# Optimization experiments

Hardware: AMD Instinct MI355X
Metric: run time of the kernel (lower is better)

Reference implementation:

```python
import jax, jax.numpy as jnp
import numpy as np

B, N, IN_DIM, OUT_DIM, H = 4, 2048, 1024, 1024, 16
HEAD_DIM = OUT_DIM // H  # 64


def setup_inputs() -> dict:
    key = jax.random.key(0)
    k_x, k_q, k_k, k_v, k_o = jax.random.split(key, 5)
    s = 1.0 / np.sqrt(IN_DIM)
    return {
        "x": jax.random.normal(k_x, (B, N, IN_DIM), dtype=jnp.float32),
        "w_q": jax.random.normal(k_q, (IN_DIM, OUT_DIM), dtype=jnp.float32) * s,
        "w_k": jax.random.normal(k_k, (IN_DIM, OUT_DIM), dtype=jnp.float32) * s,
        "w_v": jax.random.normal(k_v, (IN_DIM, OUT_DIM), dtype=jnp.float32) * s,
        "w_out": jax.random.normal(k_o, (OUT_DIM, OUT_DIM), dtype=jnp.float32) * s,
    }


def reference(x, w_q, w_k, w_v, w_out):
    b, n, _ = x.shape
    scale = 1.0 / jnp.sqrt(jnp.float32(HEAD_DIM))
    # QKV projections, split into heads: [b, h, n, d]
    q = (x @ w_q).reshape(b, n, H, HEAD_DIM).transpose(0, 2, 1, 3)
    k = (x @ w_k).reshape(b, n, H, HEAD_DIM).transpose(0, 2, 1, 3)
    v = (x @ w_v).reshape(b, n, H, HEAD_DIM).transpose(0, 2, 1, 3)
    # full score matrix [b, h, q, k]
    scores = jnp.einsum("bhqd,bhkd->bhqk", q, k) * scale
    # NOTE: source applies softmax over dim=1 (the HEAD axis) — reproduce exactly
    attn = jax.nn.softmax(scores, axis=1)
    # dropout p=0.0 -> identity
    ctx = jnp.einsum("bhqk,bhkd->bqhd", attn, v).reshape(b, n, OUT_DIM)
    return ctx @ w_out
```

## Files before the change

kernel.cpp:

```cpp
#include <hip/hip_runtime.h>
#include <hip/hip_bf16.h>

typedef unsigned short u16;
typedef unsigned int u32;
typedef __attribute__((ext_vector_type(8))) short short8;
typedef __attribute__((ext_vector_type(4))) float float4v;
typedef __attribute__((ext_vector_type(4))) unsigned int uint4v;

__device__ __forceinline__ u16 f2bf(float f) {
    union { float f; unsigned int u; } v; v.f = f;
    unsigned int r = v.u + 0x7fffu + ((v.u >> 16) & 1u);
    return (u16)(r >> 16);
}
__device__ __forceinline__ float bf2f(u16 h) {
    union { unsigned int u; float f; } v; v.u = ((unsigned int)h) << 16;
    return v.f;
}

__device__ __forceinline__ void gld_lds16(const u16* g, u16* l) {
    __builtin_amdgcn_global_load_lds(
        (const __attribute__((address_space(1))) u32*)g,
        (__attribute__((address_space(3))) u32*)l, 16, 0, 0);
}

__global__ __launch_bounds__(256) void convert_x(
    const float* __restrict__ x, u16* __restrict__ xb) {
    int i = (blockIdx.x * 256 + threadIdx.x) * 8;
    float4v a = *(const float4v*)&x[i];
    float4v b = *(const float4v*)&x[i + 4];
    u16 tmp[8] __attribute__((aligned(16)));
#pragma unroll
    for (int j = 0; j < 4; ++j) { tmp[j] = f2bf(a[j]); tmp[4 + j] = f2bf(b[j]); }
    *(uint4v*)&xb[i] = *(uint4v*)tmp;
}

__global__ __launch_bounds__(256) void transpose_w(
    const float* __restrict__ w0, const float* __restrict__ w1,
    const float* __restrict__ w2, const float* __restrict__ w3,
    u16* __restrict__ o0, u16* __restrict__ o1,
    u16* __restrict__ o2, u16* __restrict__ o3) {
    __shared__ u16 t[32][33];
    int z = blockIdx.z;
    const float* w = (z == 0) ? w0 : (z == 1) ? w1 : (z == 2) ? w2 : w3;
    u16* o         = (z == 0) ? o0 : (z == 1) ? o1 : (z == 2) ? o2 : o3;
    int bx = blockIdx.x * 32;
    int by = blockIdx.y * 32;
    int x = threadIdx.x, y = threadIdx.y;
#pragma unroll
    for (int i = 0; i < 4; ++i)
        t[y + i * 8][x] = f2bf(w[(size_t)(by + y + i * 8) * 1024 + bx + x]);
    __syncthreads();
#pragma unroll
    for (int i = 0; i < 4; ++i)
        o[(size_t)(bx + y + i * 8) * 1024 + by + x] = t[x][y + i * 8];
}

__global__ __launch_bounds__(256) void gemm_bt(
    const u16* __restrict__ A, const u16* __restrict__ Bt,
    void* __restrict__ Cout, int M, int N, int K, int mode) {
    __shared__ __attribute__((aligned(16))) u16 As[128 * 32];
    __shared__ __attribute__((aligned(16))) u16 Bs[128 * 32];
    const int tid = threadIdx.x;
    const int m0 = blockIdx.y * 128;
    const int n0 = blockIdx.x * 128;
    const int wid = tid >> 6;
    const int lane = tid & 63;
    const int ln = lane & 15, kq = lane >> 4;
    const int wm = (wid >> 1) * 64, wn = (wid & 1) * 64;

    float4v acc[4][4] = {};
    for (int k0 = 0; k0 < K; k0 += 32) {
#pragma unroll
        for (int i = 0; i < 2; ++i) {
            int chunk = tid + i * 256;
            int row = chunk >> 2, cg = chunk & 3;
            u16* lA = &As[(size_t)(i * 256 + wid * 64) * 8];
            u16* lB = &Bs[(size_t)(i * 256 + wid * 64) * 8];
            gld_lds16(&A[(size_t)(m0 + row) * K + k0 + cg * 8], lA);
            gld_lds16(&Bt[(size_t)(n0 + row) * K + k0 + cg * 8], lB);
        }
        __syncthreads();
        short8 af[4], bfr[4];
#pragma unroll
        for (int mt = 0; mt < 4; ++mt)
            af[mt] = *(const short8*)&As[(wm + mt * 16 + ln) * 32 + kq * 8];
#pragma unroll
        for (int nt = 0; nt < 4; ++nt)
            bfr[nt] = *(const short8*)&Bs[(wn + nt * 16 + ln) * 32 + kq * 8];
#pragma unroll
        for (int mt = 0; mt < 4; ++mt)
#pragma unroll
            for (int nt = 0; nt < 4; ++nt)
                acc[mt][nt] = __builtin_amdgcn_mfma_f32_16x16x32_bf16(
                    af[mt], bfr[nt], acc[mt][nt], 0, 0, 0);
        __syncthreads();
    }
    if (mode == 0) {
        u16* C = (u16*)Cout;
#pragma unroll
        for (int mt = 0; mt < 4; ++mt)
#pragma unroll
            for (int nt = 0; nt < 4; ++nt)
#pragma unroll
                for (int r = 0; r < 4; ++r) {
                    int row = m0 + wm + mt * 16 + kq * 4 + r;
                    int col = n0 + wn + nt * 16 + ln;
                    C[(size_t)row * N + col] = f2bf(acc[mt][nt][r]);
                }
    } else if (mode == 1) {
        u16* C = (u16*)Cout;
#pragma unroll
        for (int mt = 0; mt < 4; ++mt)
#pragma unroll
            for (int nt = 0; nt < 4; ++nt)
#pragma unroll
                for (int r = 0; r < 4; ++r) {
                    int t = m0 + wm + mt * 16 + kq * 4 + r;
                    int col = n0 + wn + nt * 16 + ln;
                    int b = t >> 11, n = t & 2047;
                    C[((size_t)(b * 1024 + col)) * 2048 + n] = f2bf(acc[mt][nt][r]);
                }
    } else {
        float* C = (float*)Cout;
#pragma unroll
        for (int mt = 0; mt < 4; ++mt)
#pragma unroll
            for (int nt = 0; nt < 4; ++nt)
#pragma unroll
                for (int r = 0; r < 4; ++r) {
                    int row = m0 + wm + mt * 16 + kq * 4 + r;
                    int col = n0 + wn + nt * 16 + ln;
                    C[(size_t)row * N + col] = acc[mt][nt][r];
                }
    }
}

__global__ __launch_bounds__(1024) void attn_kernel(
    const u16* qb, const u16* __restrict__ kb,
    const u16* __restrict__ vt, u16* cb) {
    __shared__ __attribute__((aligned(16))) u16 E[2][16 * 32 * 40];
    __shared__ float Di[32 * 36];

    const int b = blockIdx.y;
    const int q0 = blockIdx.x * 32;
    const int tid = threadIdx.x;
    const int wid = tid >> 6, lane = tid & 63;
    const int ln = lane & 15, kq = lane >> 4;
    const int h = wid;

    short8 aq[2][2];
#pragma unroll
    for (int mt = 0; mt < 2; ++mt)
#pragma unroll
        for (int kc = 0; kc < 2; ++kc)
            aq[mt][kc] = *(const short8*)&qb[
                (size_t)(b * 2048 + q0 + mt * 16 + ln) * 1024 +
                h * 64 + kc * 32 + kq * 8];

    float4v cacc[2][4] = {};

#pragma unroll 1
    for (int kt = 0; kt < 2048; kt += 32) {
        const int cur = (kt >> 5) & 1;
        short8 bk[2][2];
        short8 bv[4];
#pragma unroll
        for (int kc = 0; kc < 2; ++kc)
#pragma unroll
            for (int nt = 0; nt < 2; ++nt)
                bk[kc][nt] = *(const short8*)&kb[
                    (size_t)(b * 2048 + kt + nt * 16 + ln) * 1024 +
                    h * 64 + kc * 32 + kq * 8];
#pragma unroll
        for (int nt = 0; nt < 4; ++nt)
            bv[nt] = *(const short8*)&vt[
                (size_t)(b * 1024 + h * 64 + nt * 16 + ln) * 2048 + kt + kq * 8];

        float4v sacc[2][2] = {};
#pragma unroll
        for (int kc = 0; kc < 2; ++kc)
#pragma unroll
            for (int mt = 0; mt < 2; ++mt)
#pragma unroll
                for (int nt = 0; nt < 2; ++nt)
                    sacc[mt][nt] = __builtin_amdgcn_mfma_f32_16x16x32_bf16(
                        aq[mt][kc], bk[kc][nt], sacc[mt][nt], 0, 0, 0);

#pragma unroll
        for (int mt = 0; mt < 2; ++mt)
#pragma unroll
            for (int nt = 0; nt < 2; ++nt)
#pragma unroll
                for (int r = 0; r < 4; ++r) {
                    float s = sacc[mt][nt][r] * 0.18033688f;
                    E[cur][(h * 32 + mt * 16 + kq * 4 + r) * 40 + nt * 16 + ln] =
                        f2bf(exp2f(fminf(s, 115.0f)));
                }
        __syncthreads();

        {
            int q = tid >> 5, kk = tid & 31;
            float d = 0.f;
#pragma unroll
            for (int hh = 0; hh < 16; ++hh)
                d += bf2f(E[cur][(hh * 32 + q) * 40 + kk]);
            Di[q * 36 + kk] = __builtin_amdgcn_rcpf(d);
        }
        __syncthreads();

        short8 ap[2];
#pragma unroll
        for (int mt = 0; mt < 2; ++mt) {
            const u16* ep = &E[cur][(h * 32 + mt * 16 + ln) * 40 + kq * 8];
            const float* dp = &Di[(mt * 16 + ln) * 36 + kq * 8];
            u16 tmp[8] __attribute__((aligned(16)));
#pragma unroll
            for (int j = 0; j < 8; ++j)
                tmp[j] = f2bf(bf2f(ep[j]) * dp[j]);
            ap[mt] = *(short8*)tmp;
        }
#pragma unroll
        for (int nt = 0; nt < 4; ++nt)
#pragma unroll
            for (int mt = 0; mt < 2; ++mt)
                cacc[mt][nt] = __builtin_amdgcn_mfma_f32_16x16x32_bf16(
                    ap[mt], bv[nt], cacc[mt][nt], 0, 0, 0);
    }

#pragma unroll
    for (int mt = 0; mt < 2; ++mt)
#pragma unroll
        for (int nt = 0; nt < 4; ++nt)
#pragma unroll
            for (int r = 0; r < 4; ++r) {
                int row = b * 2048 + q0 + mt * 16 + kq * 4 + r;
                int col = h * 64 + nt * 16 + ln;
                cb[(size_t)row * 1024 + col] = f2bf(cacc[mt][nt][r]);
            }
}

extern "C" void kernel_launch(void* const* d_in, const int* in_sizes, int n_in,
                              void* d_out, int out_size, void* d_ws, size_t ws_size,
                              hipStream_t stream) {
    const float* x   = (const float*)d_in[0];
    const float* w_q = (const float*)d_in[1];
    const float* w_k = (const float*)d_in[2];
    const float* w_v = (const float*)d_in[3];
    const float* w_o = (const float*)d_in[4];

    char* ws = (char*)d_ws;
    const size_t SZ_W   = (size_t)1024 * 1024 * 2;
    const size_t SZ_TOK = (size_t)8192 * 1024 * 2;
    u16* x_bf  = (u16*)(ws);
    u16* wtq   = (u16*)(ws + SZ_TOK);
    u16* wtk   = (u16*)(ws + SZ_TOK + SZ_W);
    u16* wtv   = (u16*)(ws + SZ_TOK + 2 * SZ_W);
    u16* wto   = (u16*)(ws + SZ_TOK + 3 * SZ_W);
    u16* q_buf = (u16*)(ws + SZ_TOK + 4 * SZ_W);
    u16* k_buf  = (u16*)d_out;
    u16* vt_buf = (u16*)d_out + (size_t)8192 * 1024;

    convert_x<<<4096, 256, 0, stream>>>(x, x_bf);

    transpose_w<<<dim3(32, 32, 4), dim3(32, 8), 0, stream>>>(
        w_q, w_k, w_v, w_o, wtq, wtk, wtv, wto);

    gemm_bt<<<dim3(8, 64), 256, 0, stream>>>(x_bf, wtq, q_buf, 8192, 1024, 1024, 0);
    gemm_bt<<<dim3(8, 64), 256, 0, stream>>>(x_bf, wtk, k_buf, 8192, 1024, 1024, 0);
    gemm_bt<<<dim3(8, 64), 256, 0, stream>>>(x_bf, wtv, vt_buf, 8192, 1024, 1024, 1);

    attn_kernel<<<dim3(64, 4), 1024, 0, stream>>>(q_buf, k_buf, vt_buf, q_buf);

    gemm_bt<<<dim3(8, 64), 256, 0, stream>>>(q_buf, wto, d_out, 8192, 1024, 1024, 2);
}
```

Baseline: 509.2 us.

## Fuse QKV projections into one GEMM and split attention keys across blocks

The three separate Q/K/V projection GEMMs become one launch over a concatenated transposed weight, with the epilogue routing columns to Q, K or transposed V. The attention kernel now splits the key range in half, launching 512 blocks instead of 256 to fill more compute units. The two partial context results are combined through bf16-pair atomic CAS loops into a zeroed buffer that reuses the x workspace. This adds a memset, CAS contention, and a second bf16 rounding of the partial sums, which could change accuracy.

```diff
diff --git a/kernel.cpp b/kernel.cpp
--- a/kernel.cpp
+++ b/kernel.cpp
@@ -37,12 +37,11 @@
 __global__ __launch_bounds__(256) void transpose_w(
     const float* __restrict__ w0, const float* __restrict__ w1,
     const float* __restrict__ w2, const float* __restrict__ w3,
-    u16* __restrict__ o0, u16* __restrict__ o1,
-    u16* __restrict__ o2, u16* __restrict__ o3) {
+    u16* __restrict__ wqkv, u16* __restrict__ wout) {
     __shared__ u16 t[32][33];
     int z = blockIdx.z;
     const float* w = (z == 0) ? w0 : (z == 1) ? w1 : (z == 2) ? w2 : w3;
-    u16* o         = (z == 0) ? o0 : (z == 1) ? o1 : (z == 2) ? o2 : o3;
+    u16* o = (z == 3) ? wout : (wqkv + (size_t)z * 1024 * 1024);
     int bx = blockIdx.x * 32;
     int by = blockIdx.y * 32;
     int x = threadIdx.x, y = threadIdx.y;
@@ -55,9 +54,9 @@
         o[(size_t)(bx + y + i * 8) * 1024 + by + x] = t[x][y + i * 8];
 }
 
-__global__ __launch_bounds__(256) void gemm_bt(
+__global__ __launch_bounds__(256) void gemm_qkv(
     const u16* __restrict__ A, const u16* __restrict__ Bt,
-    void* __restrict__ Cout, int M, int N, int K, int mode) {
+    u16* __restrict__ Q, u16* __restrict__ Kb, u16* __restrict__ Vt, int K) {
     __shared__ __attribute__((aligned(16))) u16 As[128 * 32];
     __shared__ __attribute__((aligned(16))) u16 Bs[128 * 32];
     const int tid = threadIdx.x;
@@ -95,8 +94,9 @@
                     af[mt], bfr[nt], acc[mt][nt], 0, 0, 0);
         __syncthreads();
     }
-    if (mode == 0) {
-        u16* C = (u16*)Cout;
+    if (n0 < 2048) {
+        u16* C = (n0 < 1024) ? Q : Kb;
+        int nb = n0 & 1023;
 #pragma unroll
         for (int mt = 0; mt < 4; ++mt)
 #pragma unroll
@@ -104,11 +104,10 @@
 #pragma unroll
                 for (int r = 0; r < 4; ++r) {
                     int row = m0 + wm + mt * 16 + kq * 4 + r;
-                    int col = n0 + wn + nt * 16 + ln;
-                    C[(size_t)row * N + col] = f2bf(acc[mt][nt][r]);
+                    int col = nb + wn + nt * 16 + ln;
+                    C[(size_t)row * 1024 + col] = f2bf(acc[mt][nt][r]);
                 }
-    } else if (mode == 1) {
-        u16* C = (u16*)Cout;
+    } else {
 #pragma unroll
         for (int mt = 0; mt < 4; ++mt)
 #pragma unroll
@@ -116,33 +115,75 @@
 #pragma unroll
                 for (int r = 0; r < 4; ++r) {
                     int t = m0 + wm + mt * 16 + kq * 4 + r;
-                    int col = n0 + wn + nt * 16 + ln;
+                    int col = (n0 - 2048) + wn + nt * 16 + ln;
                     int b = t >> 11, n = t & 2047;
-                    C[((size_t)(b * 1024 + col)) * 2048 + n] = f2bf(acc[mt][nt][r]);
-                }
-    } else {
-        float* C = (float*)Cout;
-#pragma unroll
-        for (int mt = 0; mt < 4; ++mt)
-#pragma unroll
-            for (int nt = 0; nt < 4; ++nt)
-#pragma unroll
-                for (int r = 0; r < 4; ++r) {
-                    int row = m0 + wm + mt * 16 + kq * 4 + r;
-                    int col = n0 + wn + nt * 16 + ln;
-                    C[(size_t)row * N + col] = acc[mt][nt][r];
+                    Vt[((size_t)(b * 1024 + col)) * 2048 + n] = f2bf(acc[mt][nt][r]);
                 }
     }
 }
 
+__global__ __launch_bounds__(256) void gemm_out(
+    const u16* __restrict__ A, const u16* __restrict__ Bt,
+    float* __restrict__ C, int N, int K) {
+    __shared__ __attribute__((aligned(16))) u16 As[128 * 32];
+    __shared__ __attribute__((aligned(16))) u16 Bs[128 * 32];
+    const int tid = threadIdx.x;
+    const int m0 = blockIdx.y * 128;
+    const int n0 = blockIdx.x * 128;
+    const int wid = tid >> 6;
+    const int lane = tid & 63;
+    const int ln = lane & 15, kq = lane >> 4;
+    const int wm = (wid >> 1) * 64, wn = (wid & 1) * 64;
+
+    float4v acc[4][4] = {};
+    for (int k0 = 0; k0 < K; k0 += 32) {
+#pragma unroll
+        for (int i = 0; i < 2; ++i) {
+            int chunk = tid + i * 256;
+            int row = chunk >> 2, cg = chunk & 3;
+            u16* lA = &As[(size_t)(i * 256 + wid * 64) * 8];
+            u16* lB = &Bs[(size_t)(i * 256 + wid * 64) * 8];
+            gld_lds16(&A[(size_t)(m0 + row) * K + k0 + cg * 8], lA);
+            gld_lds16(&Bt[(size_t)(n0 + row) * K + k0 + cg * 8], lB);
+        }
+        __syncthreads();
+        short8 af[4], bfr[4];
+#pragma unroll
+        for (int mt = 0; mt < 4; ++mt)
+            af[mt] = *(const short8*)&As[(wm + mt * 16 + ln) * 32 + kq * 8];
+#pragma unroll
+        for (int nt = 0; nt < 4; ++nt)
+            bfr[nt] = *(const short8*)&Bs[(wn + nt * 16 + ln) * 32 + kq * 8];
+#pragma unroll
+        for (int mt = 0; mt < 4; ++mt)
+#pragma unroll
+            for (int nt = 0; nt < 4; ++nt)
+                acc[mt][nt] = __builtin_amdgcn_mfma_f32_16x16x32_bf16(
+                    af[mt], bfr[nt], acc[mt][nt], 0, 0, 0);
+        __syncthreads();
+    }
+#pragma unroll
+    for (int mt = 0; mt < 4; ++mt)
+#pragma unroll
+        for (int nt = 0; nt < 4; ++nt)
+#pragma unroll
+            for (int r = 0; r < 4; ++r) {
+                int row = m0 + wm + mt * 16 + kq * 4 + r;
+                int col = n0 + wn + nt * 16 + ln;
+                C[(size_t)row * N + col] = acc[mt][nt][r];
+            }
+}
+
 __global__ __launch_bounds__(1024) void attn_kernel(
-    const u16* qb, const u16* __restrict__ kb,
-    const u16* __restrict__ vt, u16* cb) {
+    const u16* __restrict__ qb, const u16* __restrict__ kb,
+    const u16* __restrict__ vt, u32* __restrict__ ctx) {
     __shared__ __attribute__((aligned(16))) u16 E[2][16 * 32 * 40];
     __shared__ float Di[32 * 36];
 
-    const int b = blockIdx.y;
-    const int q0 = blockIdx.x * 32;
+    const int bid = blockIdx.x;
+    const int b  = (bid >> 1) & 3;
+    const int kh = bid & 1;
+    const int q0 = (bid >> 3) * 32;
     const int tid = threadIdx.x;
     const int wid = tid >> 6, lane = tid & 63;
     const int ln = lane & 15, kq = lane >> 4;
@@ -159,8 +200,9 @@
 
     float4v cacc[2][4] = {};
 
+    const int kbeg = kh * 1024, kend = kbeg + 1024;
 #pragma unroll 1
-    for (int kt = 0; kt < 2048; kt += 32) {
+    for (int kt = kbeg; kt < kend; kt += 32) {
         const int cur = (kt >> 5) & 1;
         short8 bk[2][2];
         short8 bv[4];
@@ -233,9 +275,23 @@
         for (int nt = 0; nt < 4; ++nt)
 #pragma unroll
             for (int r = 0; r < 4; ++r) {
-                int row = b * 2048 + q0 + mt * 16 + kq * 4 + r;
-                int col = h * 64 + nt * 16 + ln;
-                cb[(size_t)row * 1024 + col] = f2bf(cacc[mt][nt][r]);
+                float v = cacc[mt][nt][r];
+                float v2 = __shfl_xor(v, 1);
+                if ((lane & 1) == 0) {
+                    int row = b * 2048 + q0 + mt * 16 + kq * 4 + r;
+                    int col = h * 64 + nt * 16 + ln;
+                    u32* addr = &ctx[((size_t)row * 1024 + col) >> 1];
+                    u32 old = __hip_atomic_load(addr, __ATOMIC_RELAXED,
+                                                __HIP_MEMORY_SCOPE_AGENT);
+                    u32 assumed;
+                    do {
+                        assumed = old;
+                        float lo = bf2f((u16)(assumed & 0xffff)) + v;
+                        float hi = bf2f((u16)(assumed >> 16)) + v2;
+                        u32 nv = ((u32)f2bf(hi) << 16) | (u32)f2bf(lo);
+                        old = atomicCAS(addr, assumed, nv);
+                    } while (old != assumed);
+                }
             }
 }
 
@@ -249,27 +305,25 @@
     const float* w_o = (const float*)d_in[4];
 
     char* ws = (char*)d_ws;
-    const size_t SZ_W   = (size_t)1024 * 1024 * 2;
     const size_t SZ_TOK = (size_t)8192 * 1024 * 2;
-    u16* x_bf  = (u16*)(ws);
-    u16* wtq   = (u16*)(ws + SZ_TOK);
-    u16* wtk   = (u16*)(ws + SZ_TOK + SZ_W);
-    u16* wtv   = (u16*)(ws + SZ_TOK + 2 * SZ_W);
-    u16* wto   = (u16*)(ws + SZ_TOK + 3 * SZ_W);
-    u16* q_buf = (u16*)(ws + SZ_TOK + 4 * SZ_W);
+    u16* x_bf   = (u16*)(ws);
+    u16* ctx    = (u16*)(ws);
+    u16* wqkv_t = (u16*)(ws + SZ_TOK);
+    u16* wto    = (u16*)(ws + SZ_TOK + (size_t)3 * 1024 * 1024 * 2);
+    u16* q_buf  = (u16*)(ws + SZ_TOK + (size_t)4 * 1024 * 1024 * 2);
     u16* k_buf  = (u16*)d_out;
     u16* vt_buf = (u16*)d_out + (size_t)8192 * 1024;
 
     convert_x<<<4096, 256, 0, stream>>>(x, x_bf);
 
     transpose_w<<<dim3(32, 32, 4), dim3(32, 8), 0, stream>>>(
-        w_q, w_k, w_v, w_o, wtq, wtk, wtv, wto);
-
-    gemm_bt<<<dim3(8, 64), 256, 0, stream>>>(x_bf, wtq, q_buf, 8192, 1024, 1024, 0);
-    gemm_bt<<<dim3(8, 64), 256, 0, stream>>>(x_bf, wtk, k_buf, 8192, 1024, 1024, 0);
-    gemm_bt<<<dim3(8, 64), 256, 0, stream>>>(x_bf, wtv, vt_buf, 8192, 1024, 1024, 1);
-
-    attn_kernel<<<dim3(64, 4), 1024, 0, stream>>>(q_buf, k_buf, vt_buf, q_buf);
-
-    gemm_bt<<<dim3(8, 64), 256, 0, stream>>>(q_buf, wto, d_out, 8192, 1024, 1024, 2);
-}
+        w_q, w_k, w_v, w_o, wqkv_t, wto);
+
+    gemm_qkv<<<dim3(24, 64), 256, 0, stream>>>(
+        x_bf, wqkv_t, q_buf, k_buf, vt_buf, 1024);
+
+    hipMemsetAsync(ctx, 0, SZ_TOK, stream);
+    attn_kernel<<<512, 1024, 0, stream>>>(q_buf, k_buf, vt_buf, (u32*)ctx);
+
+    gemm_out<<<dim3(8, 64), 256, 0, stream>>>(ctx, wto, (float*)d_out, 1024, 1024);
+}
```

After: 547.4 us. 1.07x slower.
